# Kernel optimization log

Measured on AMD Instinct MI355X. Metric: run time of the kernel, lower is better.

## Reference

```python
import jax, jax.numpy as jnp
import numpy as np

HIDDEN = 768
NUM_HEADS = 12
HEAD_SIZE = HIDDEN // NUM_HEADS
LN_EPS = 1e-5


def setup_inputs() -> dict:
    key = jax.random.key(0)
    ks = jax.random.split(key, 10)
    B, S, H = 2, 4096, HIDDEN
    std = 1.0 / np.sqrt(H)
    inp = {
        "hidden_states": jax.random.normal(ks[0], (B, S, H), dtype=jnp.float32),
        "attention_mask": jnp.ones((B, S), dtype=jnp.float32),
        "Wq": jax.random.normal(ks[1], (H, H), dtype=jnp.float32) * std,
        "bq": jnp.zeros((H,), dtype=jnp.float32),
        "Wk": jax.random.normal(ks[2], (H, H), dtype=jnp.float32) * std,
        "bk": jnp.zeros((H,), dtype=jnp.float32),
        "Wv": jax.random.normal(ks[3], (H, H), dtype=jnp.float32) * std,
        "bv": jnp.zeros((H,), dtype=jnp.float32),
        "Wo": jax.random.normal(ks[4], (H, H), dtype=jnp.float32) * std,
        "bo": jnp.zeros((H,), dtype=jnp.float32),
        "ln_gamma": jnp.ones((H,), dtype=jnp.float32),
        "ln_beta": jnp.zeros((H,), dtype=jnp.float32),
    }
    return inp


def _split_heads(x):
    # [B, S, H] -> [B, nH, S, hd]
    B, S, _ = x.shape
    return x.reshape(B, S, NUM_HEADS, HEAD_SIZE).transpose(0, 2, 1, 3)


def reference(hidden_states, attention_mask, Wq, bq, Wk, bk, Wv, bv, Wo, bo, ln_gamma, ln_beta):
    # QKV projections (torch Linear: x @ W.T + b; here W is stored as [in, out])
    q = _split_heads(hidden_states @ Wq + bq)
    k = _split_heads(hidden_states @ Wk + bk)
    v = _split_heads(hidden_states @ Wv + bv)

    scores = jnp.einsum("bhqd,bhkd->bhqk", q, k) / jnp.sqrt(jnp.float32(HEAD_SIZE))
    # additive mask: (1 - mask) * -10000, broadcast over heads and query positions
    scores = scores + (1.0 - attention_mask)[:, None, None, :] * -10000.0
    probs = jax.nn.softmax(scores, axis=-1)  # dropout_prob = 0 -> identity

    ctx = jnp.einsum("bhqk,bhkd->bhqd", probs, v)
    B, _, S, _ = ctx.shape
    ctx = ctx.transpose(0, 2, 1, 3).reshape(B, S, HIDDEN)

    out = ctx @ Wo + bo
    resid = out + hidden_states
    mu = jnp.mean(resid, axis=-1, keepdims=True)
    var = jnp.var(resid, axis=-1, keepdims=True)
    return (resid - mu) * jax.lax.rsqrt(var + LN_EPS) * ln_gamma + ln_beta
```

## Files before the change

kernel.cpp:

```cpp
#include <hip/hip_runtime.h>
#include <hip/hip_bf16.h>

#define HID 768
#define NHEADS 12
#define HDIM 64
#define SEQ 4096
#define BB 2
#define MTOT (BB * SEQ)

typedef __attribute__((ext_vector_type(8))) short bf16x8;
typedef __attribute__((ext_vector_type(16))) float f32x16;

#define LOG2E 1.4426950408889634f

__device__ inline unsigned pack2bf(float a, float b) {
    __hip_bfloat162 h = __float22bfloat162_rn(float2{a, b});
    return *(unsigned*)&h;
}

__global__ __launch_bounds__(256) void cast_x_kernel(
    const float* __restrict__ X, __hip_bfloat16* __restrict__ Xb)
{
    const size_t i = ((size_t)blockIdx.x * 256 + threadIdx.x) * 8;
    const float4 x0 = *(const float4*)(X + i);
    const float4 x1 = *(const float4*)(X + i + 4);
    unsigned u[4];
    u[0] = pack2bf(x0.x, x0.y);
    u[1] = pack2bf(x0.z, x0.w);
    u[2] = pack2bf(x1.x, x1.y);
    u[3] = pack2bf(x1.z, x1.w);
    *(uint4*)(Xb + i) = *(uint4*)u;
}

__global__ __launch_bounds__(256) void pack_w_kernel(
    const float* __restrict__ Wq, const float* __restrict__ Wk,
    const float* __restrict__ Wv, const float* __restrict__ Wo,
    __hip_bfloat16* __restrict__ Wt)
{
    const int z = blockIdx.z;
    const float* __restrict__ W = (z == 0) ? Wq : (z == 1) ? Wk : (z == 2) ? Wv : Wo;
    const int in0  = blockIdx.x * 64;
    const int out0 = blockIdx.y * 64;
    const int t = threadIdx.x;

    __shared__ float T[64][65];
#pragma unroll
    for (int i = 0; i < 4; ++i) {
        const int idx = t + 256 * i;
        const int row = idx >> 4;
        const int c4  = (idx & 15) << 2;
        const float4 v = *(const float4*)(W + (size_t)(in0 + row) * HID + out0 + c4);
        T[row][c4 + 0] = v.x; T[row][c4 + 1] = v.y;
        T[row][c4 + 2] = v.z; T[row][c4 + 3] = v.w;
    }
    __syncthreads();

    const int o  = t >> 2;
    const int cb = (t & 3) << 4;
    __hip_bfloat16 tmp[16];
#pragma unroll
    for (int k = 0; k < 16; ++k)
        tmp[k] = __float2bfloat16(T[cb + k][o]);
    __hip_bfloat16* __restrict__ dst =
        Wt + (size_t)(z * HID + out0 + o) * HID + in0 + cb;
    *(uint4*)(dst)     = *(uint4*)(&tmp[0]);
    *(uint4*)(dst + 8) = *(uint4*)(&tmp[8]);
}

__global__ __launch_bounds__(256) void qkv_mfma_kernel(
    const __hip_bfloat16* __restrict__ Xb, const __hip_bfloat16* __restrict__ Wt,
    const float* __restrict__ bq, const float* __restrict__ bk,
    const float* __restrict__ bv,
    __hip_bfloat16* __restrict__ Qo, __hip_bfloat16* __restrict__ Ko,
    __hip_bfloat16* __restrict__ Vo)
{
    const int nblk = blockIdx.x;
    const int z  = nblk / 6;
    const int f0 = (nblk % 6) * 128;
    const int n0 = nblk * 128;
    const int m0 = blockIdx.y * 128;

    const float* __restrict__ bias = (z == 0) ? bq : (z == 1) ? bk : bv;

    const int t    = threadIdx.x;
    const int w    = t >> 6;
    const int lane = t & 63;
    const int col  = lane & 31;
    const int g    = lane >> 5;
    const int wm   = w & 1;
    const int wn   = w >> 1;

    __shared__ __hip_bfloat16 smem[2 * 128 * 72];
    __hip_bfloat16 (*As)[72] = (__hip_bfloat16(*)[72])smem;
    __hip_bfloat16 (*Bs)[72] = (__hip_bfloat16(*)[72])(smem + 128 * 72);

    f32x16 acc[2][2];
#pragma unroll
    for (int mt = 0; mt < 2; ++mt)
#pragma unroll
        for (int nt = 0; nt < 2; ++nt)
#pragma unroll
            for (int r = 0; r < 16; ++r) acc[mt][nt][r] = 0.f;

    for (int k0 = 0; k0 < HID; k0 += 64) {
        __syncthreads();
#pragma unroll
        for (int i = 0; i < 4; ++i) {
            const int idx = t + 256 * i;
            const int row = idx >> 3;
            const int c8  = (idx & 7) << 3;
            *(uint4*)&As[row][c8] = *(const uint4*)(Xb + (size_t)(m0 + row) * HID + k0 + c8);
            *(uint4*)&Bs[row][c8] = *(const uint4*)(Wt + (size_t)(n0 + row) * HID + k0 + c8);
        }
        __syncthreads();
#pragma unroll
        for (int kh = 0; kh < 4; ++kh) {
            const int ko = 16 * kh + 8 * g;
            const bf16x8 a0 = *(const bf16x8*)&As[64 * wm + col][ko];
            const bf16x8 a1 = *(const bf16x8*)&As[64 * wm + 32 + col][ko];
            const bf16x8 b0 = *(const bf16x8*)&Bs[64 * wn + col][ko];
            const bf16x8 b1 = *(const bf16x8*)&Bs[64 * wn + 32 + col][ko];
            acc[0][0] = __builtin_amdgcn_mfma_f32_32x32x16_bf16(a0, b0, acc[0][0], 0, 0, 0);
            acc[0][1] = __builtin_amdgcn_mfma_f32_32x32x16_bf16(a0, b1, acc[0][1], 0, 0, 0);
            acc[1][0] = __builtin_amdgcn_mfma_f32_32x32x16_bf16(a1, b0, acc[1][0], 0, 0, 0);
            acc[1][1] = __builtin_amdgcn_mfma_f32_32x32x16_bf16(a1, b1, acc[1][1], 0, 0, 0);
        }
    }

    if (z < 2) {
        __hip_bfloat16* __restrict__ Out = (z == 0) ? Qo : Ko;
        const int h = (f0 >> 6) + wn;
#pragma unroll
        for (int mt = 0; mt < 2; ++mt)
#pragma unroll
            for (int nt = 0; nt < 2; ++nt) {
                const int d = 32 * nt + col;
                const float bsv = bias[f0 + 64 * wn + d];
#pragma unroll
                for (int r = 0; r < 16; ++r) {
                    const int m = m0 + 64 * wm + 32 * mt + (r & 3) + 8 * (r >> 2) + 4 * g;
                    const int b = m >> 12;
                    const int s = m & (SEQ - 1);
                    Out[(((size_t)(b * NHEADS + h)) * SEQ + s) * HDIM + d] =
                        __float2bfloat16(acc[mt][nt][r] + bsv);
                }
            }
    } else {
        __syncthreads();
        __hip_bfloat16 (*Ts)[136] = (__hip_bfloat16(*)[136])smem;
#pragma unroll
        for (int mt = 0; mt < 2; ++mt)
#pragma unroll
            for (int nt = 0; nt < 2; ++nt) {
                const int nloc = 64 * wn + 32 * nt + col;
                const float bsv = bias[f0 + nloc];
#pragma unroll
                for (int rg = 0; rg < 4; ++rg) {
                    const int mbase = 64 * wm + 32 * mt + 8 * rg + 4 * g;
                    unsigned pu[2];
                    pu[0] = pack2bf(acc[mt][nt][4 * rg + 0] + bsv,
                                    acc[mt][nt][4 * rg + 1] + bsv);
                    pu[1] = pack2bf(acc[mt][nt][4 * rg + 2] + bsv,
                                    acc[mt][nt][4 * rg + 3] + bsv);
                    *(uint2*)&Ts[nloc][mbase] = *(uint2*)pu;
                }
            }
        __syncthreads();
        const int nloc = t >> 1;
        const int half = t & 1;
        const int hh = (f0 >> 6) + (nloc >> 6);
        const int d  = nloc & 63;
        const int bb = m0 >> 12;
        const int s0 = m0 & (SEQ - 1);
        __hip_bfloat16* __restrict__ dst =
            Vo + (((size_t)(bb * NHEADS + hh)) * HDIM + d) * SEQ + s0 + 64 * half;
        const __hip_bfloat16* srcp = &Ts[nloc][64 * half];
#pragma unroll
        for (int j = 0; j < 8; ++j)
            *(uint4*)(dst + 8 * j) = *(const uint4*)(srcp + 8 * j);
    }
}

__global__ __launch_bounds__(256, 2) void attn_kernel(
    const __hip_bfloat16* __restrict__ Qb, const __hip_bfloat16* __restrict__ Kb,
    const __hip_bfloat16* __restrict__ Vt, const float* __restrict__ mask,
    __hip_bfloat16* __restrict__ Op, float* __restrict__ lp)
{
    const int bh = blockIdx.y;
    const int b  = bh / NHEADS;
    const int h  = bh - b * NHEADS;
    const int kspan = SEQ / gridDim.z;
    const int kbeg  = blockIdx.z * kspan;

    const int t    = threadIdx.x;
    const int w    = t >> 6;
    const int lane = t & 63;
    const int col  = lane & 31;
    const int g    = lane >> 5;
    const int qw   = blockIdx.x * 256 + 64 * w;

    __shared__ __hip_bfloat16 Ks[64][72];
    __shared__ __hip_bfloat16 Vts[64][72];
    __shared__ float madd[64];

    const __hip_bfloat16* __restrict__ Qh = Qb + (size_t)bh * SEQ * HDIM;
    const __hip_bfloat16* __restrict__ Kh = Kb + (size_t)bh * SEQ * HDIM;
    const __hip_bfloat16* __restrict__ Vh = Vt + (size_t)bh * HDIM * SEQ;

    bf16x8 bq[2][4];
#pragma unroll
    for (int mt = 0; mt < 2; ++mt)
#pragma unroll
        for (int kh = 0; kh < 4; ++kh)
            bq[mt][kh] = *(const bf16x8*)(Qh + (size_t)(qw + 32 * mt + col) * HDIM
                                          + 16 * kh + 8 * g);

    f32x16 O[2][2];
    float lac[2] = {0.f, 0.f};
#pragma unroll
    for (int mt = 0; mt < 2; ++mt)
#pragma unroll
        for (int dt = 0; dt < 2; ++dt)
#pragma unroll
            for (int r = 0; r < 16; ++r) O[mt][dt][r] = 0.f;

    const float kscale = 0.125f * LOG2E;

    for (int kt0 = 0; kt0 < kspan; kt0 += 64) {
        const int kt = kbeg + kt0;
        __syncthreads();
#pragma unroll
        for (int i = 0; i < 2; ++i) {
            const int idx = t + 256 * i;
            const int row = idx >> 3;
            const int c8  = (idx & 7) << 3;
            *(uint4*)&Ks[row][c8]  = *(const uint4*)(Kh + (size_t)(kt + row) * HDIM + c8);
            *(uint4*)&Vts[row][c8] = *(const uint4*)(Vh + (size_t)row * SEQ + kt + c8);
        }
        if (t < 64) madd[t] = (1.0f - mask[b * SEQ + kt + t]) * (-10000.0f * LOG2E);
        __syncthreads();

        f32x16 St[2][2];
#pragma unroll
        for (int mt = 0; mt < 2; ++mt)
#pragma unroll
            for (int nt = 0; nt < 2; ++nt)
#pragma unroll
                for (int r = 0; r < 16; ++r) St[mt][nt][r] = 0.f;

#pragma unroll
        for (int kh = 0; kh < 4; ++kh) {
            const bf16x8 ak0 = *(const bf16x8*)&Ks[col][16 * kh + 8 * g];
            const bf16x8 ak1 = *(const bf16x8*)&Ks[32 + col][16 * kh + 8 * g];
            St[0][0] = __builtin_amdgcn_mfma_f32_32x32x16_bf16(ak0, bq[0][kh], St[0][0], 0, 0, 0);
            St[1][0] = __builtin_amdgcn_mfma_f32_32x32x16_bf16(ak0, bq[1][kh], St[1][0], 0, 0, 0);
            St[0][1] = __builtin_amdgcn_mfma_f32_32x32x16_bf16(ak1, bq[0][kh], St[0][1], 0, 0, 0);
            St[1][1] = __builtin_amdgcn_mfma_f32_32x32x16_bf16(ak1, bq[1][kh], St[1][1], 0, 0, 0);
        }

#pragma unroll
        for (int mt = 0; mt < 2; ++mt) {
            unsigned g4x[2][4], g4y[2][4];
#pragma unroll
            for (int nt = 0; nt < 2; ++nt) {
#pragma unroll
                for (int b4 = 0; b4 < 4; ++b4) {
                    const float4 mm = *(const float4*)&madd[32 * nt + 8 * b4 + 4 * g];
                    const float p0 = __builtin_amdgcn_exp2f(fmaf(St[mt][nt][4 * b4 + 0], kscale, mm.x));
                    const float p1 = __builtin_amdgcn_exp2f(fmaf(St[mt][nt][4 * b4 + 1], kscale, mm.y));
                    const float p2 = __builtin_amdgcn_exp2f(fmaf(St[mt][nt][4 * b4 + 2], kscale, mm.z));
                    const float p3 = __builtin_amdgcn_exp2f(fmaf(St[mt][nt][4 * b4 + 3], kscale, mm.w));
                    lac[mt] += (p0 + p1) + (p2 + p3);
                    g4x[nt][b4] = pack2bf(p0, p1);
                    g4y[nt][b4] = pack2bf(p2, p3);
                }
            }
#pragma unroll
            for (int kh = 0; kh < 4; ++kh) {
                const int nt  = kh >> 1;
                const int khl = kh & 1;
                const unsigned lo_x = g4x[nt][2 * khl],     lo_y = g4y[nt][2 * khl];
                const unsigned hi_x = g4x[nt][2 * khl + 1], hi_y = g4y[nt][2 * khl + 1];
                const unsigned sx = g ? lo_x : hi_x;
                const unsigned sy = g ? lo_y : hi_y;
                const unsigned rx = (unsigned)__shfl_xor((int)sx, 32, 64);
                const unsigned ry = (unsigned)__shfl_xor((int)sy, 32, 64);
                union { unsigned u[4]; bf16x8 v; } au;
                if (g) { au.u[0] = rx; au.u[1] = ry; au.u[2] = hi_x; au.u[3] = hi_y; }
                else   { au.u[0] = lo_x; au.u[1] = lo_y; au.u[2] = rx; au.u[3] = ry; }
                const bf16x8 bv0 = *(const bf16x8*)&Vts[col][16 * kh + 8 * g];
                const bf16x8 bv1 = *(const bf16x8*)&Vts[32 + col][16 * kh + 8 * g];
                O[mt][0] = __builtin_amdgcn_mfma_f32_32x32x16_bf16(au.v, bv0, O[mt][0], 0, 0, 0);
                O[mt][1] = __builtin_amdgcn_mfma_f32_32x32x16_bf16(au.v, bv1, O[mt][1], 0, 0, 0);
            }
        }
    }

    const size_t opbase = (size_t)blockIdx.z * ((size_t)MTOT * HID);
#pragma unroll
    for (int mt = 0; mt < 2; ++mt) {
        const float l = lac[mt] + __shfl_xor(lac[mt], 32, 64);
        if (g == 0)
            lp[((size_t)blockIdx.z * (BB * NHEADS) + bh) * SEQ + qw + 32 * mt + col] = l;
#pragma unroll
        for (int dt = 0; dt < 2; ++dt)
#pragma unroll
            for (int r = 0; r < 16; ++r) {
                const int q = qw + 32 * mt + (r & 3) + 8 * (r >> 2) + 4 * g;
                const int d = 32 * dt + col;
                Op[opbase + ((size_t)b * SEQ + q) * HID + h * HDIM + d] =
                    __float2bfloat16(O[mt][dt][r]);
            }
    }
}

__global__ __launch_bounds__(256) void combine_kernel(
    const __hip_bfloat16* __restrict__ Op, const float* __restrict__ lp,
    __hip_bfloat16* __restrict__ Ctx, int KS)
{
    const size_t i = ((size_t)blockIdx.x * 256 + threadIdx.x) * 8;
    const int n   = (int)(i % HID);
    const int row = (int)(i / HID);
    const int h = n >> 6;
    const int b = row >> 12;
    const int q = row & (SEQ - 1);
    const int bh = b * NHEADS + h;

    float denom = 0.f;
    float o[8] = {};
    for (int kz = 0; kz < KS; ++kz) {
        denom += lp[((size_t)kz * (BB * NHEADS) + bh) * SEQ + q];
        uint4 u = *(const uint4*)(Op + (size_t)kz * ((size_t)MTOT * HID) + i);
        const __hip_bfloat16* e = (const __hip_bfloat16*)&u;
#pragma unroll
        for (int j = 0; j < 8; ++j) o[j] += __bfloat162float(e[j]);
    }
    const float inv = 1.0f / denom;
    unsigned u[4];
#pragma unroll
    for (int j = 0; j < 4; ++j)
        u[j] = pack2bf(o[2 * j] * inv, o[2 * j + 1] * inv);
    *(uint4*)(Ctx + i) = *(uint4*)u;
}

__global__ __launch_bounds__(256) void out_mfma_kernel(
    const __hip_bfloat16* __restrict__ Cb, const __hip_bfloat16* __restrict__ Wto,
    const float* __restrict__ bo, const float* __restrict__ X,
    float* __restrict__ Resid)
{
    const int n0 = blockIdx.x * 128;
    const int m0 = blockIdx.y * 128;

    const int t    = threadIdx.x;
    const int w    = t >> 6;
    const int lane = t & 63;
    const int col  = lane & 31;
    const int g    = lane >> 5;
    const int wm   = w & 1;
    const int wn   = w >> 1;

    __shared__ __hip_bfloat16 As[128][72];
    __shared__ __hip_bfloat16 Bs[128][72];

    f32x16 acc[2][2];
#pragma unroll
    for (int mt = 0; mt < 2; ++mt)
#pragma unroll
        for (int nt = 0; nt < 2; ++nt)
#pragma unroll
            for (int r = 0; r < 16; ++r) acc[mt][nt][r] = 0.f;

    for (int k0 = 0; k0 < HID; k0 += 64) {
        __syncthreads();
#pragma unroll
        for (int i = 0; i < 4; ++i) {
            const int idx = t + 256 * i;
            const int row = idx >> 3;
            const int c8  = (idx & 7) << 3;
            *(uint4*)&As[row][c8] = *(const uint4*)(Cb  + (size_t)(m0 + row) * HID + k0 + c8);
            *(uint4*)&Bs[row][c8] = *(const uint4*)(Wto + (size_t)(n0 + row) * HID + k0 + c8);
        }
        __syncthreads();
#pragma unroll
        for (int kh = 0; kh < 4; ++kh) {
            const int ko = 16 * kh + 8 * g;
            const bf16x8 a0 = *(const bf16x8*)&As[64 * wm + col][ko];
            const bf16x8 a1 = *(const bf16x8*)&As[64 * wm + 32 + col][ko];
            const bf16x8 b0 = *(const bf16x8*)&Bs[64 * wn + col][ko];
            const bf16x8 b1 = *(const bf16x8*)&Bs[64 * wn + 32 + col][ko];
            acc[0][0] = __builtin_amdgcn_mfma_f32_32x32x16_bf16(a0, b0, acc[0][0], 0, 0, 0);
            acc[0][1] = __builtin_amdgcn_mfma_f32_32x32x16_bf16(a0, b1, acc[0][1], 0, 0, 0);
            acc[1][0] = __builtin_amdgcn_mfma_f32_32x32x16_bf16(a1, b0, acc[1][0], 0, 0, 0);
            acc[1][1] = __builtin_amdgcn_mfma_f32_32x32x16_bf16(a1, b1, acc[1][1], 0, 0, 0);
        }
    }

#pragma unroll
    for (int mt = 0; mt < 2; ++mt)
#pragma unroll
        for (int nt = 0; nt < 2; ++nt) {
            const int n = n0 + 64 * wn + 32 * nt + col;
            const float bsv = bo[n];
#pragma unroll
            for (int r = 0; r < 16; ++r) {
                const int m = m0 + 64 * wm + 32 * mt + (r & 3) + 8 * (r >> 2) + 4 * g;
                Resid[(size_t)m * HID + n] = acc[mt][nt][r] + bsv + X[(size_t)m * HID + n];
            }
        }
}

__global__ __launch_bounds__(256) void ln_kernel(
    const float* __restrict__ Rin, const float* __restrict__ gamma,
    const float* __restrict__ beta, float* __restrict__ Out)
{
    const int row = blockIdx.x;
    const int t   = threadIdx.x;
    const float* __restrict__ x = Rin + (size_t)row * HID;

    const float v0 = x[t];
    const float v1 = x[t + 256];
    const float v2 = x[t + 512];
    float s  = v0 + v1 + v2;
    float s2 = v0 * v0 + v1 * v1 + v2 * v2;
#pragma unroll
    for (int off = 32; off; off >>= 1) {
        s  += __shfl_xor(s,  off, 64);
        s2 += __shfl_xor(s2, off, 64);
    }
    __shared__ float rs[4], rs2[4];
    const int w = t >> 6, lane = t & 63;
    if (lane == 0) { rs[w] = s; rs2[w] = s2; }
    __syncthreads();
    const float tot  = rs[0] + rs[1] + rs[2] + rs[3];
    const float tot2 = rs2[0] + rs2[1] + rs2[2] + rs2[3];
    const float mu   = tot * (1.0f / HID);
    const float var  = tot2 * (1.0f / HID) - mu * mu;
    const float rsig = rsqrtf(var + 1e-5f);

    float* __restrict__ y = Out + (size_t)row * HID;
    y[t]       = (v0 - mu) * rsig * gamma[t]       + beta[t];
    y[t + 256] = (v1 - mu) * rsig * gamma[t + 256] + beta[t + 256];
    y[t + 512] = (v2 - mu) * rsig * gamma[t + 512] + beta[t + 512];
}

extern "C" void kernel_launch(void* const* d_in, const int* in_sizes, int n_in,
                              void* d_out, int out_size, void* d_ws, size_t ws_size,
                              hipStream_t stream)
{
    const float* X     = (const float*)d_in[0];
    const float* mask  = (const float*)d_in[1];
    const float* Wq    = (const float*)d_in[2];
    const float* bq    = (const float*)d_in[3];
    const float* Wk    = (const float*)d_in[4];
    const float* bk    = (const float*)d_in[5];
    const float* Wv    = (const float*)d_in[6];
    const float* bv    = (const float*)d_in[7];
    const float* Wo    = (const float*)d_in[8];
    const float* bo    = (const float*)d_in[9];
    const float* gamma = (const float*)d_in[10];
    const float* beta  = (const float*)d_in[11];
    float* out = (float*)d_out;

    const size_t N = (size_t)MTOT * HID;
    const size_t WTE = (size_t)4 * HID * HID;

    char* p = (char*)d_ws;
    __hip_bfloat16* Xb  = (__hip_bfloat16*)p;  p += 2 * N;
    __hip_bfloat16* Wt  = (__hip_bfloat16*)p;  p += 2 * WTE;
    __hip_bfloat16* Qw  = (__hip_bfloat16*)p;  p += 2 * N;
    __hip_bfloat16* Kw  = (__hip_bfloat16*)p;  p += 2 * N;
    __hip_bfloat16* Vtw = (__hip_bfloat16*)p;  p += 2 * N;
    char* opb = p;
    const size_t fixed = (size_t)(opb - (char*)d_ws);

    const size_t lpsz4 = 4 * (size_t)(BB * NHEADS) * SEQ * sizeof(float);
    const int KS = (ws_size >= fixed + 4 * 2 * N + lpsz4) ? 4 : 2;

    __hip_bfloat16* Op  = (__hip_bfloat16*)opb;
    float* lpt = (float*)(opb + (size_t)KS * 2 * N);
    __hip_bfloat16* Ctxb = Xb;
    float* Rd = (float*)Kw;

    cast_x_kernel<<<(int)(N / 2048), 256, 0, stream>>>(X, Xb);
    pack_w_kernel<<<dim3(12, 12, 4), 256, 0, stream>>>(Wq, Wk, Wv, Wo, Wt);
    qkv_mfma_kernel<<<dim3(18, MTOT / 128), 256, 0, stream>>>(
        Xb, Wt, bq, bk, bv, Qw, Kw, Vtw);
    attn_kernel<<<dim3(SEQ / 256, BB * NHEADS, KS), 256, 0, stream>>>(
        Qw, Kw, Vtw, mask, Op, lpt);
    combine_kernel<<<(int)(N / 2048), 256, 0, stream>>>(Op, lpt, Ctxb, KS);
    out_mfma_kernel<<<dim3(6, MTOT / 128), 256, 0, stream>>>(
        Ctxb, Wt + (size_t)2304 * HID, bo, X, Rd);
    ln_kernel<<<MTOT, 256, 0, stream>>>(Rd, gamma, beta, out);
}
```

Baseline: 341.7 us.

## Prefetch K/V tiles into registers, precompute mask, use permlane32 swap

Moves the next K/V tile's global loads into registers issued right after the shared-memory store, so global latency overlaps the current tile's MFMA and softmax work. The additive mask is computed once for the whole key span into a larger shared array instead of once per tile. The exp/pack loop is reordered so one mask read serves both query tiles, and V fragments are loaded once per kh for both mt. Where the builtin exists, the cross-half exchange uses the gfx950 permlane32_swap instruction in place of two shuffles plus selects. The cost is more registers for the prefetch buffers, which may hurt occupancy, and 8KB of extra LDS.

```diff
diff --git a/kernel.cpp b/kernel.cpp
--- a/kernel.cpp
+++ b/kernel.cpp
@@ -181,6 +181,8 @@
     }
 }
 
+typedef __attribute__((ext_vector_type(2))) unsigned uswap2;
+
 __global__ __launch_bounds__(256, 2) void attn_kernel(
     const __hip_bfloat16* __restrict__ Qb, const __hip_bfloat16* __restrict__ Kb,
     const __hip_bfloat16* __restrict__ Vt, const float* __restrict__ mask,
@@ -201,12 +203,15 @@
 
     __shared__ __hip_bfloat16 Ks[64][72];
     __shared__ __hip_bfloat16 Vts[64][72];
-    __shared__ float madd[64];
+    __shared__ float madd[2048];
 
     const __hip_bfloat16* __restrict__ Qh = Qb + (size_t)bh * SEQ * HDIM;
     const __hip_bfloat16* __restrict__ Kh = Kb + (size_t)bh * SEQ * HDIM;
     const __hip_bfloat16* __restrict__ Vh = Vt + (size_t)bh * HDIM * SEQ;
 
+    for (int j = t; j < kspan; j += 256)
+        madd[j] = (1.0f - mask[b * SEQ + kbeg + j]) * (-10000.0f * LOG2E);
+
     bf16x8 bq[2][4];
 #pragma unroll
     for (int mt = 0; mt < 2; ++mt)
@@ -226,19 +231,26 @@
 
     const float kscale = 0.125f * LOG2E;
 
+    const int srow = t >> 3;
+    const int sc8  = (t & 7) << 3;
+    uint4 kreg[2], vreg[2];
+
+#define ATTN_LOAD(KT)                                                          \
+    kreg[0] = *(const uint4*)(Kh + (size_t)((KT) + srow) * HDIM + sc8);        \
+    kreg[1] = *(const uint4*)(Kh + (size_t)((KT) + srow + 32) * HDIM + sc8);   \
+    vreg[0] = *(const uint4*)(Vh + (size_t)srow * SEQ + (KT) + sc8);           \
+    vreg[1] = *(const uint4*)(Vh + (size_t)(srow + 32) * SEQ + (KT) + sc8);
+
+    ATTN_LOAD(kbeg);
+
     for (int kt0 = 0; kt0 < kspan; kt0 += 64) {
-        const int kt = kbeg + kt0;
-        __syncthreads();
-#pragma unroll
-        for (int i = 0; i < 2; ++i) {
-            const int idx = t + 256 * i;
-            const int row = idx >> 3;
-            const int c8  = (idx & 7) << 3;
-            *(uint4*)&Ks[row][c8]  = *(const uint4*)(Kh + (size_t)(kt + row) * HDIM + c8);
-            *(uint4*)&Vts[row][c8] = *(const uint4*)(Vh + (size_t)row * SEQ + kt + c8);
-        }
-        if (t < 64) madd[t] = (1.0f - mask[b * SEQ + kt + t]) * (-10000.0f * LOG2E);
-        __syncthreads();
+        __syncthreads();
+        *(uint4*)&Ks[srow][sc8]       = kreg[0];
+        *(uint4*)&Ks[srow + 32][sc8]  = kreg[1];
+        *(uint4*)&Vts[srow][sc8]      = vreg[0];
+        *(uint4*)&Vts[srow + 32][sc8] = vreg[1];
+        __syncthreads();
+        if (kt0 + 64 < kspan) { ATTN_LOAD(kbeg + kt0 + 64); }
 
         f32x16 St[2][2];
 #pragma unroll
@@ -258,43 +270,55 @@
             St[1][1] = __builtin_amdgcn_mfma_f32_32x32x16_bf16(ak1, bq[1][kh], St[1][1], 0, 0, 0);
         }
 
-#pragma unroll
-        for (int mt = 0; mt < 2; ++mt) {
-            unsigned g4x[2][4], g4y[2][4];
-#pragma unroll
-            for (int nt = 0; nt < 2; ++nt) {
-#pragma unroll
-                for (int b4 = 0; b4 < 4; ++b4) {
-                    const float4 mm = *(const float4*)&madd[32 * nt + 8 * b4 + 4 * g];
+        unsigned pkx[2][2][4], pky[2][2][4];
+#pragma unroll
+        for (int nt = 0; nt < 2; ++nt)
+#pragma unroll
+            for (int b4 = 0; b4 < 4; ++b4) {
+                const float4 mm = *(const float4*)&madd[kt0 + 32 * nt + 8 * b4 + 4 * g];
+#pragma unroll
+                for (int mt = 0; mt < 2; ++mt) {
                     const float p0 = __builtin_amdgcn_exp2f(fmaf(St[mt][nt][4 * b4 + 0], kscale, mm.x));
                     const float p1 = __builtin_amdgcn_exp2f(fmaf(St[mt][nt][4 * b4 + 1], kscale, mm.y));
                     const float p2 = __builtin_amdgcn_exp2f(fmaf(St[mt][nt][4 * b4 + 2], kscale, mm.z));
                     const float p3 = __builtin_amdgcn_exp2f(fmaf(St[mt][nt][4 * b4 + 3], kscale, mm.w));
                     lac[mt] += (p0 + p1) + (p2 + p3);
-                    g4x[nt][b4] = pack2bf(p0, p1);
-                    g4y[nt][b4] = pack2bf(p2, p3);
+                    pkx[mt][nt][b4] = pack2bf(p0, p1);
+                    pky[mt][nt][b4] = pack2bf(p2, p3);
                 }
             }
-#pragma unroll
-            for (int kh = 0; kh < 4; ++kh) {
-                const int nt  = kh >> 1;
-                const int khl = kh & 1;
-                const unsigned lo_x = g4x[nt][2 * khl],     lo_y = g4y[nt][2 * khl];
-                const unsigned hi_x = g4x[nt][2 * khl + 1], hi_y = g4y[nt][2 * khl + 1];
-                const unsigned sx = g ? lo_x : hi_x;
-                const unsigned sy = g ? lo_y : hi_y;
-                const unsigned rx = (unsigned)__shfl_xor((int)sx, 32, 64);
-                const unsigned ry = (unsigned)__shfl_xor((int)sy, 32, 64);
+
+#pragma unroll
+        for (int kh = 0; kh < 4; ++kh) {
+            const int nt  = kh >> 1;
+            const int khl = kh & 1;
+            const bf16x8 bv0 = *(const bf16x8*)&Vts[col][16 * kh + 8 * g];
+            const bf16x8 bv1 = *(const bf16x8*)&Vts[32 + col][16 * kh + 8 * g];
+#pragma unroll
+            for (int mt = 0; mt < 2; ++mt) {
                 union { unsigned u[4]; bf16x8 v; } au;
+#if __has_builtin(__builtin_amdgcn_permlane32_swap)
+                uswap2 sx = __builtin_amdgcn_permlane32_swap(
+                    pkx[mt][nt][2 * khl], pkx[mt][nt][2 * khl + 1], false, false);
+                uswap2 sy = __builtin_amdgcn_permlane32_swap(
+                    pky[mt][nt][2 * khl], pky[mt][nt][2 * khl + 1], false, false);
+                au.u[0] = sx[0]; au.u[1] = sy[0]; au.u[2] = sx[1]; au.u[3] = sy[1];
+#else
+                const unsigned lo_x = pkx[mt][nt][2 * khl],     lo_y = pky[mt][nt][2 * khl];
+                const unsigned hi_x = pkx[mt][nt][2 * khl + 1], hi_y = pky[mt][nt][2 * khl + 1];
+                const unsigned sxv = g ? lo_x : hi_x;
+                const unsigned syv = g ? lo_y : hi_y;
+                const unsigned rx = (unsigned)__shfl_xor((int)sxv, 32, 64);
+                const unsigned ry = (unsigned)__shfl_xor((int)syv, 32, 64);
                 if (g) { au.u[0] = rx; au.u[1] = ry; au.u[2] = hi_x; au.u[3] = hi_y; }
                 else   { au.u[0] = lo_x; au.u[1] = lo_y; au.u[2] = rx; au.u[3] = ry; }
-                const bf16x8 bv0 = *(const bf16x8*)&Vts[col][16 * kh + 8 * g];
-                const bf16x8 bv1 = *(const bf16x8*)&Vts[32 + col][16 * kh + 8 * g];
+#endif
                 O[mt][0] = __builtin_amdgcn_mfma_f32_32x32x16_bf16(au.v, bv0, O[mt][0], 0, 0, 0);
                 O[mt][1] = __builtin_amdgcn_mfma_f32_32x32x16_bf16(au.v, bv1, O[mt][1], 0, 0, 0);
             }
         }
     }
+#undef ATTN_LOAD
 
     const size_t opbase = (size_t)blockIdx.z * ((size_t)MTOT * HID);
 #pragma unroll
```

Result: slower. 397.7 us (+16.4%).
